# Kernel optimization log

Hardware: AMD Instinct MI355X
Metric: run time of the kernel (lower is better)

Reference implementation:

```python
import jax, jax.numpy as jnp
import numpy as np

B, S, E, H = 4, 2048, 2048, 16
D = E // H  # head_dim = 128


def _rotary_tables():
    # standard interleaved RoPE: pairs (2i, 2i+1) share an angle
    inv_freq = 1.0 / (10000.0 ** (np.arange(0, D, 2, dtype=np.float64) / D))
    ang = np.arange(S, dtype=np.float64)[:, None] * inv_freq[None, :]  # [S, D/2]
    ang = np.repeat(ang, 2, axis=-1)  # [S, D]
    cos = np.cos(ang).astype(np.float32)[None, None]  # [1,1,S,D]
    sin = np.sin(ang).astype(np.float32)[None, None]
    return jnp.asarray(cos), jnp.asarray(sin)


def setup_inputs() -> dict:
    key = jax.random.key(0)
    ks = jax.random.split(key, 4)
    x = jax.random.normal(ks[0], (B, S, E), jnp.float32)
    cos, sin = _rotary_tables()
    Wqkv = jax.random.normal(ks[1], (E, 3 * E), jnp.float32) * 0.02
    bqkv = jnp.zeros((3 * E,), jnp.float32)
    Wproj = jax.random.normal(ks[2], (E, E), jnp.float32) * 0.02
    bproj = jnp.zeros((E,), jnp.float32)
    return {"x": x, "rotary_cos": cos, "rotary_sin": sin,
            "Wqkv": Wqkv, "bqkv": bqkv, "Wproj": Wproj, "bproj": bproj}


def apply_rotary(t, cos, sin):
    # t: [B,H,S,D]; interleaved rotate-half: (x1,x2) -> (-x2, x1)
    x1 = t[..., 0::2]
    x2 = t[..., 1::2]
    rot = jnp.stack((-x2, x1), axis=-1).reshape(t.shape)
    return t * cos + rot * sin


def reference(x, rotary_cos, rotary_sin, Wqkv, bqkv, Wproj, bproj):
    qkv = x @ Wqkv + bqkv  # [B,S,3E]
    q, k, v = jnp.split(qkv, 3, axis=-1)
    # [B,S,E] -> [B,H,S,D]
    to_heads = lambda t: t.reshape(B, S, H, D).transpose(0, 2, 1, 3)
    q, k, v = to_heads(q), to_heads(k), to_heads(v)
    q = apply_rotary(q, rotary_cos, rotary_sin)
    k = apply_rotary(k, rotary_cos, rotary_sin)
    scale = 1.0 / jnp.sqrt(jnp.float32(D))
    scores = jnp.einsum("bhqd,bhkd->bhqk", q, k) * scale  # non-causal
    attn = jax.nn.softmax(scores, axis=-1)
    y = jnp.einsum("bhqk,bhkd->bhqd", attn, v)
    y = y.transpose(0, 2, 1, 3).reshape(B, S, E)
    out = y @ Wproj + bproj
    return out, k, v
```

## Files before the change

kernel.cpp:

```cpp
#include <hip/hip_runtime.h>


typedef unsigned short u16;
typedef unsigned int   u32;
typedef float  f32x4  __attribute__((ext_vector_type(4)));
typedef __bf16 bf16x8 __attribute__((ext_vector_type(8)));

#define B_  4
#define S_  2048
#define E_  2048
#define H_  16
#define D_  128

__device__ __forceinline__ u16 f2bf(float f) {
    union { float f; u32 u; } v; v.f = f;
    return (u16)((v.u + 0x8000u) >> 16);
}
__device__ __forceinline__ u32 pack_bf(float a, float b) {
    union { float f; u32 u; } x, y; x.f = a; y.f = b;
    return ((x.u + 0x8000u) >> 16) | ((y.u + 0x8000u) & 0xFFFF0000u);
}
__device__ __forceinline__ float bf2f(u16 h) {
    union { u32 u; float f; } v; v.u = ((u32)h) << 16; return v.f;
}

__device__ __forceinline__ void gld16(const u16* g, u16* l) {
    __builtin_amdgcn_global_load_lds(
        (const __attribute__((address_space(1))) void*)g,
        (__attribute__((address_space(3))) void*)l, 16, 0, 0);
}

__global__ __launch_bounds__(256) void xconv_kernel(
    const float* __restrict__ x, u16* __restrict__ xb)
{
    size_t g = (size_t)blockIdx.x * 256 + threadIdx.x;
    const float4* p = (const float4*)x + g * 2;
    float4 a = p[0], b = p[1];
    uint4 pk;
    pk.x = pack_bf(a.x, a.y); pk.y = pack_bf(a.z, a.w);
    pk.z = pack_bf(b.x, b.y); pk.w = pack_bf(b.z, b.w);
    ((uint4*)xb)[g] = pk;
}

__global__ __launch_bounds__(256) void wtrans_kernel(
    const float* __restrict__ W, u16* __restrict__ WT, int K, int N)
{
    __shared__ float tile[64][65];
    const int n0 = blockIdx.x * 64, k0 = blockIdx.y * 64;
    const int t = threadIdx.x;
#pragma unroll
    for (int i = 0; i < 16; ++i) {
        int idx = i * 256 + t; int r = idx >> 6, c = idx & 63;
        tile[r][c] = W[(size_t)(k0 + r) * N + n0 + c];
    }
    __syncthreads();
#pragma unroll
    for (int i = 0; i < 16; ++i) {
        int idx = i * 256 + t; int rn = idx >> 6, ck = idx & 63;
        WT[(size_t)(n0 + rn) * K + k0 + ck] = f2bf(tile[ck][rn]);
    }
}

__device__ __forceinline__ void stage_half(
    const u16* __restrict__ g, int K, u16* l, int t)
{
    const int wb = (t >> 6) << 6;
#pragma unroll
    for (int j = 0; j < 2; ++j) {
        const int idx = j * 512 + t;
        const int row = idx >> 3, c = (idx & 7) ^ (row & 7);
        gld16(g + (size_t)row * K + (c << 3),
              l + ((j * 512 + wb) << 3));
    }
}

template <int MODE>
__global__ __launch_bounds__(512, 2) void gemm_kernel(
    const u16* __restrict__ A, const u16* __restrict__ Bt,
    const float* __restrict__ bias,
    u16* __restrict__ qh, u16* __restrict__ kh, u16* __restrict__ vt,
    float* __restrict__ vout, float* __restrict__ outf,
    int N, int K)
{
    __shared__ u16 Asm[2][256 * 64];
    __shared__ u16 Bsm[2][256 * 64];

    const int t = threadIdx.x;
    const int wave = t >> 6, lane = t & 63, quad = lane >> 4, l16 = lane & 15;
    const int wr = wave >> 2, wc = wave & 3;
    const int m0 = blockIdx.y * 256, n0 = blockIdx.x * 256;
    const int NT = K >> 6;

    const int sw0 = ((quad ^ (l16 & 7)) << 3);
    const int sw1 = (((4 + quad) ^ (l16 & 7)) << 3);
    const int aRow = (wr * 128 + l16) << 6;
    const int bRow = (wc * 64 + l16) << 6;

    f32x4 acc[8][4] = {};

    const u16* Ab = A  + (size_t)m0 * K;
    const u16* Bb = Bt + (size_t)n0 * K;

    stage_half(Ab,                        K, &Asm[0][0],    t);
    stage_half(Ab + (size_t)128 * K,      K, &Asm[0][8192], t);
    stage_half(Bb,                        K, &Bsm[0][0],    t);
    stage_half(Bb + (size_t)128 * K,      K, &Bsm[0][8192], t);
    stage_half(Ab + 64,                   K, &Asm[1][0],    t);
    stage_half(Ab + (size_t)128 * K + 64, K, &Asm[1][8192], t);
    asm volatile("s_waitcnt vmcnt(4)" ::: "memory");
    __builtin_amdgcn_s_barrier();

    for (int T = 0; T < NT; ++T) {
        const int cur = T & 1, nxt = cur ^ 1;
        const int kn1 = (T + 1) << 6, kn2 = (T + 2) << 6;
        const u16* Asb = &Asm[cur][0];
        const u16* Bsb = &Bsm[cur][0];
        bf16x8 af[8], b0, b1;

#pragma unroll
        for (int mi = 0; mi < 8; ++mi)
            af[mi] = *(const bf16x8*)(Asb + aRow + mi * 1024 + sw0);
        b0 = *(const bf16x8*)(Bsb + bRow + sw0);
        b1 = *(const bf16x8*)(Bsb + bRow + 1024 + sw0);
        if (T + 1 < NT) stage_half(Bb + kn1, K, &Bsm[nxt][0], t);
        __builtin_amdgcn_s_barrier();
        asm volatile("s_waitcnt lgkmcnt(0)" ::: "memory");
        __builtin_amdgcn_s_setprio(1);
#pragma unroll
        for (int mi = 0; mi < 8; ++mi) {
            acc[mi][0] = __builtin_amdgcn_mfma_f32_16x16x32_bf16(af[mi], b0, acc[mi][0], 0, 0, 0);
            acc[mi][1] = __builtin_amdgcn_mfma_f32_16x16x32_bf16(af[mi], b1, acc[mi][1], 0, 0, 0);
        }
        __builtin_amdgcn_s_setprio(0);
        __builtin_amdgcn_s_barrier();

        b0 = *(const bf16x8*)(Bsb + bRow + 2048 + sw0);
        b1 = *(const bf16x8*)(Bsb + bRow + 3072 + sw0);
        if (T + 1 < NT) stage_half(Bb + (size_t)128 * K + kn1, K, &Bsm[nxt][8192], t);
        __builtin_amdgcn_s_barrier();
        asm volatile("s_waitcnt lgkmcnt(0)" ::: "memory");
        __builtin_amdgcn_s_setprio(1);
#pragma unroll
        for (int mi = 0; mi < 8; ++mi) {
            acc[mi][2] = __builtin_amdgcn_mfma_f32_16x16x32_bf16(af[mi], b0, acc[mi][2], 0, 0, 0);
            acc[mi][3] = __builtin_amdgcn_mfma_f32_16x16x32_bf16(af[mi], b1, acc[mi][3], 0, 0, 0);
        }
        __builtin_amdgcn_s_setprio(0);
        __builtin_amdgcn_s_barrier();

#pragma unroll
        for (int mi = 0; mi < 8; ++mi)
            af[mi] = *(const bf16x8*)(Asb + aRow + mi * 1024 + sw1);
        b0 = *(const bf16x8*)(Bsb + bRow + sw1);
        b1 = *(const bf16x8*)(Bsb + bRow + 1024 + sw1);
        __builtin_amdgcn_s_barrier();
        asm volatile("s_waitcnt lgkmcnt(0)" ::: "memory");
        __builtin_amdgcn_s_setprio(1);
#pragma unroll
        for (int mi = 0; mi < 8; ++mi) {
            acc[mi][0] = __builtin_amdgcn_mfma_f32_16x16x32_bf16(af[mi], b0, acc[mi][0], 0, 0, 0);
            acc[mi][1] = __builtin_amdgcn_mfma_f32_16x16x32_bf16(af[mi], b1, acc[mi][1], 0, 0, 0);
        }
        __builtin_amdgcn_s_setprio(0);
        __builtin_amdgcn_s_barrier();

        b0 = *(const bf16x8*)(Bsb + bRow + 2048 + sw1);
        b1 = *(const bf16x8*)(Bsb + bRow + 3072 + sw1);
        if (T + 2 < NT) {
            stage_half(Ab + kn2,                   K, &Asm[cur][0],    t);
            stage_half(Ab + (size_t)128 * K + kn2, K, &Asm[cur][8192], t);
        }
        __builtin_amdgcn_s_barrier();
        asm volatile("s_waitcnt lgkmcnt(0)" ::: "memory");
        __builtin_amdgcn_s_setprio(1);
#pragma unroll
        for (int mi = 0; mi < 8; ++mi) {
            acc[mi][2] = __builtin_amdgcn_mfma_f32_16x16x32_bf16(af[mi], b0, acc[mi][2], 0, 0, 0);
            acc[mi][3] = __builtin_amdgcn_mfma_f32_16x16x32_bf16(af[mi], b1, acc[mi][3], 0, 0, 0);
        }
        __builtin_amdgcn_s_setprio(0);
        if (T + 2 < NT) { asm volatile("s_waitcnt vmcnt(4)" ::: "memory"); }
        else            { asm volatile("s_waitcnt vmcnt(0)" ::: "memory"); }
        __builtin_amdgcn_s_barrier();
    }

    if constexpr (MODE == 0) {
        const int sel = n0 >> 11;
        const int b   = m0 >> 11, sb = m0 & 2047;
#pragma unroll
        for (int ni = 0; ni < 4; ++ni) {
            const int dg = (n0 & 2047) + wc * 64 + ni * 16 + l16;
            const int h = dg >> 7, d = dg & 127;
            const float bv = bias[n0 + wc * 64 + ni * 16 + l16];
            const size_t hb = ((size_t)(b * H_ + h)) * S_ * D_;
#pragma unroll
            for (int mi = 0; mi < 8; ++mi) {
                const int s0 = sb + wr * 128 + mi * 16 + quad * 4;
                float v0 = acc[mi][ni][0] + bv, v1 = acc[mi][ni][1] + bv;
                float v2 = acc[mi][ni][2] + bv, v3 = acc[mi][ni][3] + bv;
                size_t base = hb + (size_t)s0 * D_ + d;
                if (sel < 2) {
                    u16* dst = sel ? kh : qh;
                    dst[base]        = f2bf(v0); dst[base + D_]    = f2bf(v1);
                    dst[base + 2*D_] = f2bf(v2); dst[base + 3*D_]  = f2bf(v3);
                } else {
                    vout[base] = v0; vout[base + D_] = v1;
                    vout[base + 2*D_] = v2; vout[base + 3*D_] = v3;
                    uint2 pk; pk.x = pack_bf(v0, v1); pk.y = pack_bf(v2, v3);
                    *(uint2*)(vt + ((size_t)(b * H_ + h) * D_ + d) * S_ + s0) = pk;
                }
            }
        }
    } else {
#pragma unroll
        for (int ni = 0; ni < 4; ++ni) {
            const int col = n0 + wc * 64 + ni * 16 + l16;
            const float bv = bias[col];
#pragma unroll
            for (int mi = 0; mi < 8; ++mi) {
                const int row0 = m0 + wr * 128 + mi * 16 + quad * 4;
#pragma unroll
                for (int r = 0; r < 4; ++r)
                    outf[(size_t)(row0 + r) * N + col] = acc[mi][ni][r] + bv;
            }
        }
    }
}

__global__ __launch_bounds__(256) void rotary_kernel(
    u16* __restrict__ q, u16* __restrict__ k, float* __restrict__ kout,
    const float* __restrict__ cosT, const float* __restrict__ sinT)
{
    const int g = blockIdx.x * 256 + threadIdx.x;
    const int d0 = (g & 15) << 3;
    const int srow = g >> 4;
    const int s = srow & (S_ - 1);
    const size_t base = (size_t)srow * D_ + d0;

    uint4 qv = *(const uint4*)(q + base);
    uint4 kv = *(const uint4*)(k + base);
    float cc[8], ss[8];
    *(float4*)(cc)     = *(const float4*)(cosT + s * D_ + d0);
    *(float4*)(cc + 4) = *(const float4*)(cosT + s * D_ + d0 + 4);
    *(float4*)(ss)     = *(const float4*)(sinT + s * D_ + d0);
    *(float4*)(ss + 4) = *(const float4*)(sinT + s * D_ + d0 + 4);
    const u16* qp = (const u16*)&qv; const u16* kp = (const u16*)&kv;
    float qo[8], ko[8];
#pragma unroll
    for (int i = 0; i < 4; ++i) {
        float q1 = bf2f(qp[2*i]), q2 = bf2f(qp[2*i+1]);
        float k1 = bf2f(kp[2*i]), k2 = bf2f(kp[2*i+1]);
        qo[2*i]   = q1 * cc[2*i]   - q2 * ss[2*i];
        qo[2*i+1] = q2 * cc[2*i+1] + q1 * ss[2*i+1];
        ko[2*i]   = k1 * cc[2*i]   - k2 * ss[2*i];
        ko[2*i+1] = k2 * cc[2*i+1] + k1 * ss[2*i+1];
    }
    const float qs_ = 0.08838834764831845f * 1.4426950408889634f;
    uint4 qpk, kpk;
    u32* qq = (u32*)&qpk; u32* kq = (u32*)&kpk;
#pragma unroll
    for (int i = 0; i < 4; ++i) {
        qq[i] = pack_bf(qo[2*i] * qs_, qo[2*i+1] * qs_);
        kq[i] = pack_bf(ko[2*i], ko[2*i+1]);
    }
    *(uint4*)(q + base) = qpk;
    *(uint4*)(k + base) = kpk;
    *(float4*)(kout + base)     = make_float4(ko[0], ko[1], ko[2], ko[3]);
    *(float4*)(kout + base + 4) = make_float4(ko[4], ko[5], ko[6], ko[7]);
}

#define KSWZ(row, c) ((row) * 128 + (((c) ^ ((row) & 7)) << 3))
#define VSWZ(d, c)   ((d) * 64 + (((c) ^ ((d) & 7)) << 3))
#define PSWZ(qr, c)  ((qr) * 64 + (((c) ^ ((qr) & 7)) << 3))

__global__ __launch_bounds__(256, 4) void attn_kernel(
    const u16* __restrict__ qh, const u16* __restrict__ kh,
    const u16* __restrict__ vt, u16* __restrict__ yb)
{
    __shared__ u16 Ks[64 * 128];
    __shared__ u16 Vs[128 * 64];
    __shared__ u16 Ps[4 * 16 * 64];

    const int t = threadIdx.x, wave = t >> 6, lane = t & 63;
    const int quad = lane >> 4, l16 = lane & 15;
    const int bh = blockIdx.y, q0 = blockIdx.x * 64;
    const u16* kb = kh + (size_t)bh * S_ * D_;
    const u16* vb = vt + (size_t)bh * D_ * S_;
    u16* Pw = Ps + wave * (16 * 64);

    bf16x8 qf[4];
    {
        const u16* qp = qh + ((size_t)bh * S_ + q0 + wave * 16 + l16) * D_ + quad * 8;
#pragma unroll
        for (int kk = 0; kk < 4; ++kk) qf[kk] = *(const bf16x8*)(qp + kk * 32);
    }

    f32x4 o[8] = {};
    float m_r = -1e30f, l_r = 0.f;

    for (int k0 = 0; k0 < S_; k0 += 64) {
        __syncthreads();
#pragma unroll
        for (int i = 0; i < 4; ++i) {
            int idx = i * 256 + t;
            {
                int row = idx >> 4, c = (idx & 15) ^ (row & 7);
                gld16(kb + (size_t)(k0 + row) * D_ + (c << 3),
                      Ks + ((i * 256 + wave * 64) << 3));
            }
            {
                int d = idx >> 3, c = (idx & 7) ^ (d & 7);
                gld16(vb + (size_t)d * S_ + k0 + (c << 3),
                      Vs + ((i * 256 + wave * 64) << 3));
            }
        }
        __syncthreads();

        f32x4 sc[4] = {};
#pragma unroll
        for (int kk = 0; kk < 4; ++kk) {
#pragma unroll
            for (int nt = 0; nt < 4; ++nt) {
                bf16x8 kf = *(const bf16x8*)(Ks + KSWZ(nt * 16 + l16, kk * 4 + quad));
                sc[nt] = __builtin_amdgcn_mfma_f32_16x16x32_bf16(kf, qf[kk], sc[nt], 0, 0, 0);
            }
        }
        float mx = sc[0][0];
#pragma unroll
        for (int nt = 0; nt < 4; ++nt)
#pragma unroll
            for (int r = 0; r < 4; ++r) mx = fmaxf(mx, sc[nt][r]);
        mx = fmaxf(mx, __shfl_xor(mx, 16));
        mx = fmaxf(mx, __shfl_xor(mx, 32));
        float mn = fmaxf(m_r, mx);
        float alpha = exp2f(m_r - mn);
        m_r = mn;
        float rs = 0.f;
#pragma unroll
        for (int nt = 0; nt < 4; ++nt)
#pragma unroll
            for (int r = 0; r < 4; ++r) {
                float p = exp2f(sc[nt][r] - mn);
                sc[nt][r] = p; rs += p;
            }
        rs += __shfl_xor(rs, 16);
        rs += __shfl_xor(rs, 32);
        l_r = l_r * alpha + rs;
        float af4[4];
#pragma unroll
        for (int r = 0; r < 4; ++r) af4[r] = __shfl(alpha, quad * 4 + r);
#pragma unroll
        for (int dt = 0; dt < 8; ++dt)
#pragma unroll
            for (int r = 0; r < 4; ++r) o[dt][r] *= af4[r];

#pragma unroll
        for (int nt = 0; nt < 4; ++nt) {
            int key0 = nt * 16 + quad * 4;
            int chunk = key0 >> 3, sub = key0 & 7;
            uint2 pk;
            pk.x = pack_bf(sc[nt][0], sc[nt][1]);
            pk.y = pack_bf(sc[nt][2], sc[nt][3]);
            *(uint2*)(Pw + PSWZ(l16, chunk) + sub) = pk;
        }
#pragma unroll
        for (int kk2 = 0; kk2 < 2; ++kk2) {
            bf16x8 pf = *(const bf16x8*)(Pw + PSWZ(l16, kk2 * 4 + quad));
#pragma unroll
            for (int dt = 0; dt < 8; ++dt) {
                bf16x8 vf = *(const bf16x8*)(Vs + VSWZ(dt * 16 + l16, kk2 * 4 + quad));
                o[dt] = __builtin_amdgcn_mfma_f32_16x16x32_bf16(pf, vf, o[dt], 0, 0, 0);
            }
        }
    }
    float lf[4];
#pragma unroll
    for (int r = 0; r < 4; ++r) {
        float lv = __shfl(l_r, quad * 4 + r);
        lf[r] = __builtin_amdgcn_rcpf(lv);
    }
    const int b = bh >> 4, h = bh & 15;
#pragma unroll
    for (int dt = 0; dt < 8; ++dt) {
        int d = h * D_ + dt * 16 + l16;
#pragma unroll
        for (int r = 0; r < 4; ++r) {
            int s = q0 + wave * 16 + quad * 4 + r;
            yb[(size_t)(b * S_ + s) * E_ + d] = f2bf(o[dt][r] * lf[r]);
        }
    }
}

extern "C" void kernel_launch(void* const* d_in, const int* in_sizes, int n_in,
                              void* d_out, int out_size, void* d_ws, size_t ws_size,
                              hipStream_t stream)
{
    (void)in_sizes; (void)n_in; (void)out_size; (void)ws_size;
    const float* x     = (const float*)d_in[0];
    const float* cosT  = (const float*)d_in[1];
    const float* sinT  = (const float*)d_in[2];
    const float* Wqkv  = (const float*)d_in[3];
    const float* bqkv  = (const float*)d_in[4];
    const float* Wproj = (const float*)d_in[5];
    const float* bproj = (const float*)d_in[6];

    float* out  = (float*)d_out;
    float* kout = out  + (size_t)B_ * S_ * E_;
    float* vout = kout + (size_t)B_ * S_ * E_;

    u16* wqkvT  = (u16*)d_ws;
    u16* wprojT = wqkvT  + (size_t)12582912;
    u16* qh     = wprojT + (size_t)4194304;
    u16* kh     = qh     + (size_t)16777216;
    u16* vt     = kh     + (size_t)16777216;
    u16* yb     = vt     + (size_t)16777216;
    u16* xb     = yb;

    xconv_kernel<<<8192, 256, 0, stream>>>(x, xb);
    wtrans_kernel<<<dim3(96, 32), 256, 0, stream>>>(Wqkv, wqkvT, 2048, 6144);
    wtrans_kernel<<<dim3(32, 32), 256, 0, stream>>>(Wproj, wprojT, 2048, 2048);
    gemm_kernel<0><<<dim3(24, 32), 512, 0, stream>>>(
        xb, wqkvT, bqkv, qh, kh, vt, vout, nullptr, 6144, 2048);
    rotary_kernel<<<8192, 256, 0, stream>>>(qh, kh, kout, cosT, sinT);
    attn_kernel<<<dim3(32, 64), 256, 0, stream>>>(qh, kh, vt, yb);
    gemm_kernel<1><<<dim3(8, 32), 512, 0, stream>>>(
        yb, wprojT, bproj, nullptr, nullptr, nullptr, nullptr, out, 2048, 2048);
}
```

Measured before the change: 843.9 us.

## Add lazy softmax rescaling, XCD-aware block mapping, hw bf16 pack, MFMA priority

```diff
diff --git a/kernel.cpp b/kernel.cpp
--- a/kernel.cpp
+++ b/kernel.cpp
@@ -22,6 +22,11 @@
 }
 __device__ __forceinline__ float bf2f(u16 h) {
     union { u32 u; float f; } v; v.u = ((u32)h) << 16; return v.f;
+}
+__device__ __forceinline__ u32 cvtpk_bf16(float a, float b) {
+    u32 r;
+    asm("v_cvt_pk_bf16_f32 %0, %1, %2" : "=v"(r) : "v"(a), "v"(b));
+    return r;
 }
 
 __device__ __forceinline__ void gld16(const u16* g, u16* l) {
@@ -283,7 +288,10 @@
 
     const int t = threadIdx.x, wave = t >> 6, lane = t & 63;
     const int quad = lane >> 4, l16 = lane & 15;
-    const int bh = blockIdx.y, q0 = blockIdx.x * 64;
+    const int bid = blockIdx.x;
+    const int jj = bid >> 3;
+    const int bh = (bid & 7) * 8 + (jj >> 5);
+    const int q0 = (jj & 31) << 6;
     const u16* kb = kh + (size_t)bh * S_ * D_;
     const u16* vb = vt + (size_t)bh * D_ * S_;
     u16* Pw = Ps + wave * (16 * 64);
@@ -317,6 +325,7 @@
         __syncthreads();
 
         f32x4 sc[4] = {};
+        __builtin_amdgcn_s_setprio(1);
 #pragma unroll
         for (int kk = 0; kk < 4; ++kk) {
 #pragma unroll
@@ -325,44 +334,54 @@
                 sc[nt] = __builtin_amdgcn_mfma_f32_16x16x32_bf16(kf, qf[kk], sc[nt], 0, 0, 0);
             }
         }
-        float mx = sc[0][0];
-#pragma unroll
-        for (int nt = 0; nt < 4; ++nt)
-#pragma unroll
-            for (int r = 0; r < 4; ++r) mx = fmaxf(mx, sc[nt][r]);
+        __builtin_amdgcn_s_setprio(0);
+
+        float mx = fmaxf(sc[0][0], sc[0][1]);
+        mx = fmaxf(fmaxf(mx, sc[0][2]), sc[0][3]);
+        mx = fmaxf(fmaxf(mx, sc[1][0]), sc[1][1]);
+        mx = fmaxf(fmaxf(mx, sc[1][2]), sc[1][3]);
+        mx = fmaxf(fmaxf(mx, sc[2][0]), sc[2][1]);
+        mx = fmaxf(fmaxf(mx, sc[2][2]), sc[2][3]);
+        mx = fmaxf(fmaxf(mx, sc[3][0]), sc[3][1]);
+        mx = fmaxf(fmaxf(mx, sc[3][2]), sc[3][3]);
         mx = fmaxf(mx, __shfl_xor(mx, 16));
         mx = fmaxf(mx, __shfl_xor(mx, 32));
-        float mn = fmaxf(m_r, mx);
-        float alpha = exp2f(m_r - mn);
-        m_r = mn;
-        float rs = 0.f;
-#pragma unroll
-        for (int nt = 0; nt < 4; ++nt)
-#pragma unroll
-            for (int r = 0; r < 4; ++r) {
-                float p = exp2f(sc[nt][r] - mn);
-                sc[nt][r] = p; rs += p;
-            }
+        if (!__all(mx - m_r <= 8.0f)) {
+            float mn = fmaxf(m_r, mx);
+            float alpha = exp2f(m_r - mn);
+            m_r = mn;
+            l_r *= alpha;
+            float af4[4];
+#pragma unroll
+            for (int r = 0; r < 4; ++r) af4[r] = __shfl(alpha, quad * 4 + r);
+#pragma unroll
+            for (int dt = 0; dt < 8; ++dt)
+#pragma unroll
+                for (int r = 0; r < 4; ++r) o[dt][r] *= af4[r];
+        }
+        float rsp[4];
+#pragma unroll
+        for (int nt = 0; nt < 4; ++nt) {
+#pragma unroll
+            for (int r = 0; r < 4; ++r)
+                sc[nt][r] = exp2f(sc[nt][r] - m_r);
+            rsp[nt] = (sc[nt][0] + sc[nt][1]) + (sc[nt][2] + sc[nt][3]);
+        }
+        float rs = (rsp[0] + rsp[1]) + (rsp[2] + rsp[3]);
         rs += __shfl_xor(rs, 16);
         rs += __shfl_xor(rs, 32);
-        l_r = l_r * alpha + rs;
-        float af4[4];
-#pragma unroll
-        for (int r = 0; r < 4; ++r) af4[r] = __shfl(alpha, quad * 4 + r);
-#pragma unroll
-        for (int dt = 0; dt < 8; ++dt)
-#pragma unroll
-            for (int r = 0; r < 4; ++r) o[dt][r] *= af4[r];
+        l_r += rs;
 
 #pragma unroll
         for (int nt = 0; nt < 4; ++nt) {
             int key0 = nt * 16 + quad * 4;
             int chunk = key0 >> 3, sub = key0 & 7;
             uint2 pk;
-            pk.x = pack_bf(sc[nt][0], sc[nt][1]);
-            pk.y = pack_bf(sc[nt][2], sc[nt][3]);
+            pk.x = cvtpk_bf16(sc[nt][0], sc[nt][1]);
+            pk.y = cvtpk_bf16(sc[nt][2], sc[nt][3]);
             *(uint2*)(Pw + PSWZ(l16, chunk) + sub) = pk;
         }
+        __builtin_amdgcn_s_setprio(1);
 #pragma unroll
         for (int kk2 = 0; kk2 < 2; ++kk2) {
             bf16x8 pf = *(const bf16x8*)(Pw + PSWZ(l16, kk2 * 4 + quad));
@@ -372,6 +391,7 @@
                 o[dt] = __builtin_amdgcn_mfma_f32_16x16x32_bf16(pf, vf, o[dt], 0, 0, 0);
             }
         }
+        __builtin_amdgcn_s_setprio(0);
     }
     float lf[4];
 #pragma unroll
@@ -422,7 +442,7 @@
     gemm_kernel<0><<<dim3(24, 32), 512, 0, stream>>>(
         xb, wqkvT, bqkv, qh, kh, vt, vout, nullptr, 6144, 2048);
     rotary_kernel<<<8192, 256, 0, stream>>>(qh, kh, kout, cosT, sinT);
-    attn_kernel<<<dim3(32, 64), 256, 0, stream>>>(qh, kh, vt, yb);
+    attn_kernel<<<2048, 256, 0, stream>>>(qh, kh, vt, yb);
     gemm_kernel<1><<<dim3(8, 32), 512, 0, stream>>>(
         yb, wprojT, bproj, nullptr, nullptr, nullptr, nullptr, out, 2048, 2048);
 }
```

Result: no change. 828.9 us (-1.8%).
